# Optimization experiments

Measured on AMD Instinct MI355X. Metric: run time of the kernel, lower is better.

## Reference

```python
import jax, jax.numpy as jnp
import numpy as np

D = 64        # inner_feature_len (dim)
HID = 128     # hidden_channels of the edge MLP
NCONV = 2     # n_conv
STEPS = 3     # Set2Set processing_steps
NSEG = 128    # number of graphs in the batch


def setup_inputs() -> dict:
    key = jax.random.key(0)
    ks = jax.random.split(key, 30)
    N, E, FN, FE = 10000, 64000, 92, 41
    s = 0.05
    p = lambda i, shape: jax.random.normal(ks[i], shape, jnp.float32) * s
    return {
        "x": jax.random.normal(ks[0], (N, FN), jnp.float32),
        "edge_attr": jax.random.uniform(ks[1], (E, FE), dtype=jnp.float32),
        "lin0_w": p(2, (D, FN)), "lin0_b": p(3, (D,)),
        "nn1_w": p(4, (HID, FE)), "nn1_b": p(5, (HID,)),
        "nn2_w": p(6, (D * D, HID)), "nn2_b": p(7, (D * D,)),
        "root_w": p(8, (D, D)), "conv_b": p(9, (D,)),
        "gru_w_ih": p(10, (3 * D, D)), "gru_w_hh": p(11, (3 * D, D)),
        "gru_b_ih": p(12, (3 * D,)), "gru_b_hh": p(13, (3 * D,)),
        "lstm_w_ih": p(14, (4 * D, 2 * D)), "lstm_w_hh": p(15, (4 * D, D)),
        "lstm_b_ih": p(16, (4 * D,)), "lstm_b_hh": p(17, (4 * D,)),
        "lin1_w": p(18, (D, 2 * D)), "lin1_b": p(19, (D,)),
        "lin2_w": p(20, (1, D)), "lin2_b": p(21, (1,)),
        "edge_index": jax.random.randint(ks[22], (2, E), 0, N, dtype=jnp.int32),
        "batch": jnp.sort(jax.random.randint(ks[23], (N,), 0, NSEG, dtype=jnp.int32)),
    }


def _gru_step(m, h, w_ih, w_hh, b_ih, b_hh):
    # torch GRU gate order: r, z, n
    gi = m @ w_ih.T + b_ih
    gh = h @ w_hh.T + b_hh
    r = jax.nn.sigmoid(gi[:, :D] + gh[:, :D])
    z = jax.nn.sigmoid(gi[:, D:2 * D] + gh[:, D:2 * D])
    n = jnp.tanh(gi[:, 2 * D:] + r * gh[:, 2 * D:])
    return (1.0 - z) * n + z * h


def _forward(x, edge_attr, lin0_w, lin0_b, nn1_w, nn1_b, nn2_w, nn2_b, root_w, conv_b,
             gru_w_ih, gru_w_hh, gru_b_ih, gru_b_hh, lstm_w_ih, lstm_w_hh, lstm_b_ih,
             lstm_b_hh, lin1_w, lin1_b, lin2_w, lin2_b, edge_index, batch):
    N = x.shape[0]
    src, dst = edge_index[0], edge_index[1]

    # Edge-conditioned weight matrices: [E, D, D] (dominant intermediate)
    We = (jax.nn.relu(edge_attr @ nn1_w.T + nn1_b) @ nn2_w.T + nn2_b).reshape(-1, D, D)
    deg = jnp.clip(jax.ops.segment_sum(jnp.ones_like(src, jnp.float32), dst, num_segments=N), 1.0, None)

    out = jax.nn.relu(x @ lin0_w.T + lin0_b)   # [N, D]
    h = out                                     # GRU hidden (num_layers=1)
    for _ in range(NCONV):
        # NNConv: gather -> per-edge matmul -> scatter-mean, plus root transform + bias
        msg = jnp.einsum('ei,eio->eo', out[src], We)                 # [E, D]
        agg = jax.ops.segment_sum(msg, dst, num_segments=N) / deg[:, None]
        m = jax.nn.relu(agg + out @ root_w.T + conv_b)
        h = _gru_step(m, h, gru_w_ih, gru_w_hh, gru_b_ih, gru_b_hh)
        out = h

    # Set2Set pooling (LSTM-attention readout)
    q_star = jnp.zeros((NSEG, 2 * D), x.dtype)
    hl = jnp.zeros((NSEG, D), x.dtype)
    cl = jnp.zeros((NSEG, D), x.dtype)
    for _ in range(STEPS):
        g = q_star @ lstm_w_ih.T + lstm_b_ih + hl @ lstm_w_hh.T + lstm_b_hh
        i = jax.nn.sigmoid(g[:, :D])
        f = jax.nn.sigmoid(g[:, D:2 * D])
        gg = jnp.tanh(g[:, 2 * D:3 * D])
        o = jax.nn.sigmoid(g[:, 3 * D:])
        cl = f * cl + i * gg
        hl = o * jnp.tanh(cl)
        q = hl                                   # [NSEG, D]
        e = jnp.sum(out * q[batch], axis=-1)     # [N]
        mmax = jax.ops.segment_max(e, batch, num_segments=NSEG)
        a = jnp.exp(e - mmax[batch])
        denom = jax.ops.segment_sum(a, batch, num_segments=NSEG)
        a = a / denom[batch]
        r = jax.ops.segment_sum(a[:, None] * out, batch, num_segments=NSEG)  # [NSEG, D]
        q_star = jnp.concatenate([q, r], axis=1)

    y = jax.nn.relu(q_star @ lin1_w.T + lin1_b) @ lin2_w.T + lin2_b
    return y.reshape(-1)


def reference(x, edge_attr, lin0_w, lin0_b, nn1_w, nn1_b, nn2_w, nn2_b, root_w, conv_b,
              gru_w_ih, gru_w_hh, gru_b_ih, gru_b_hh, lstm_w_ih, lstm_w_hh, lstm_b_ih,
              lstm_b_hh, lin1_w, lin1_b, lin2_w, lin2_b, edge_index, batch):
    return _forward(x, edge_attr, lin0_w, lin0_b, nn1_w, nn1_b, nn2_w, nn2_b, root_w,
                    conv_b, gru_w_ih, gru_w_hh, gru_b_ih, gru_b_hh, lstm_w_ih, lstm_w_hh,
                    lstm_b_ih, lstm_b_hh, lin1_w, lin1_b, lin2_w, lin2_b, edge_index, batch)
```

## Files before the change

### kernel.cpp

```cpp
#include <hip/hip_runtime.h>
#include <hip/hip_bf16.h>
#include <math.h>

#define DD 64
#define HIDC 128
#define FN 92
#define FE 41
#define S2CAP 192

typedef unsigned short u16;
typedef short bf16x8 __attribute__((ext_vector_type(8)));
typedef float f32x4 __attribute__((ext_vector_type(4)));

__device__ __forceinline__ float sigmoidf_(float x){ return 1.f/(1.f+expf(-x)); }

__device__ __forceinline__ u16 f2bf(float v){
  union { float f; unsigned u; } x; x.f = v;
  unsigned r = x.u + 0x7fff + ((x.u >> 16) & 1);
  return (u16)(r >> 16);
}
__device__ __forceinline__ float bf2f(u16 v){
  union { float f; unsigned u; } x; x.u = ((unsigned)v) << 16;
  return x.f;
}
__device__ __forceinline__ void split_bf(float v, u16& h, u16& l){
  h = f2bf(v); l = f2bf(v - bf2f(h));
}

__global__ void k_pack(const float* __restrict__ lin0_w, const float* __restrict__ nn1_w,
                       const float* __restrict__ root_w, const float* __restrict__ gwih,
                       const float* __restrict__ gwhh, const float* __restrict__ lwih,
                       const float* __restrict__ lwhh, const float* __restrict__ lin1_w,
                       float* __restrict__ lin0T, float* __restrict__ nn1T,
                       float* __restrict__ rootT, float* __restrict__ wihT,
                       float* __restrict__ whhT, float* __restrict__ lwihT,
                       float* __restrict__ lwhhT, float* __restrict__ lin1T)
{
  int idx = blockIdx.x*blockDim.x + threadIdx.x;
  if (idx < 92*64){ int k=idx/64, o=idx%64; lin0T[k*64+o] = lin0_w[o*92+k]; return; } idx -= 92*64;
  if (idx < 41*128){ int k=idx/128, h=idx%128; nn1T[k*128+h] = nn1_w[h*41+k]; return; } idx -= 41*128;
  if (idx < 64*64){ int i=idx/64, o=idx%64; rootT[i*64+o] = root_w[o*64+i]; return; } idx -= 64*64;
  if (idx < 64*192){ int i=idx/192, g=idx%192; wihT[i*192+g] = gwih[g*64+i]; return; } idx -= 64*192;
  if (idx < 64*192){ int i=idx/192, g=idx%192; whhT[i*192+g] = gwhh[g*64+i]; return; } idx -= 64*192;
  if (idx < 128*256){ int j=idx/256, t=idx%256; lwihT[j*256+t] = lwih[t*128+j]; return; } idx -= 128*256;
  if (idx < 64*256){ int j=idx/256, t=idx%256; lwhhT[j*256+t] = lwhh[t*64+j]; return; } idx -= 64*256;
  if (idx < 128*64){ int j=idx/64, t=idx%64; lin1T[j*64+t] = lin1_w[t*128+j]; return; }
}

__global__ void k_pack_b2(const float* __restrict__ nn2_w,
                          u16* __restrict__ BhT, u16* __restrict__ BlT){
  int idx = blockIdx.x*256 + threadIdx.x;
  if (idx >= 524288) return;
  int i  = idx & 63;
  int ho = (idx >> 6) & 4095;
  int c  = idx >> 18;
  int h = ho >> 6, o = ho & 63;
  float v = nn2_w[(size_t)(i*64+o)*128 + c*64 + h];
  u16 hi, lo; split_bf(v, hi, lo);
  BhT[idx] = hi; BlT[idx] = lo;
}

__global__ void k_pack_b1(const float* __restrict__ nn1_w,
                          u16* __restrict__ BT1h, u16* __restrict__ BT1l){
  int idx = blockIdx.x*256 + threadIdx.x;
  if (idx >= 8192) return;
  int h = idx >> 6, k = idx & 63;
  float v = (k < FE) ? nn1_w[(size_t)h*FE + k] : 0.f;
  u16 hi, lo; split_bf(v, hi, lo);
  BT1h[idx] = hi; BT1l[idx] = lo;
}

__global__ void k_split_ea(const float* __restrict__ ea, const int* __restrict__ sortedE,
                           u16* __restrict__ eaH, u16* __restrict__ eaL, int E){
  int idx = blockIdx.x*256 + threadIdx.x;
  if (idx >= E*64) return;
  int ew = idx >> 6, k = idx & 63;
  int e = sortedE[ew];
  float v = (k < FE) ? ea[(size_t)e*FE + k] : 0.f;
  u16 hi, lo; split_bf(v, hi, lo);
  eaH[idx] = hi; eaL[idx] = lo;
}

__global__ __launch_bounds__(256) void k_node_mlp(const float* __restrict__ x,
    const float* __restrict__ lin0T, const float* __restrict__ lin0_b,
    const float* __restrict__ nn2_b,
    float* __restrict__ out, u16* __restrict__ outH, u16* __restrict__ outL,
    float* __restrict__ bterm, int N)
{
  __shared__ float xs[4][FN];
  int base = blockIdx.x*4;
  for (int i=threadIdx.x; i<4*FN; i+=256){
    int n = base + i/FN;
    xs[i/FN][i%FN] = (n<N) ? x[(size_t)n*FN + i%FN] : 0.f;
  }
  __syncthreads();
  int ln = threadIdx.x>>6, o = threadIdx.x&63;
  int n = base+ln;
  if (n>=N) return;
  float acc = lin0_b[o];
  #pragma unroll 4
  for (int k=0;k<FN;k++) acc = fmaf(xs[ln][k], lin0T[k*64+o], acc);
  float v = fmaxf(acc, 0.f);
  out[(size_t)n*64+o] = v;
  u16 hi, lo; split_bf(v, hi, lo);
  outH[(size_t)n*64+o] = hi;
  outL[(size_t)n*64+o] = lo;
  float bt = 0.f;
  #pragma unroll 8
  for (int i=0;i<64;i++) bt = fmaf(__shfl(v, i, 64), nn2_b[i*64+o], bt);
  bterm[(size_t)n*64+o] = bt;
}

__global__ void k_count(const int* __restrict__ dst, const int* __restrict__ src,
                        float* __restrict__ deg, int* __restrict__ scnt, int E){
  int e = blockIdx.x*blockDim.x + threadIdx.x;
  if (e < E){
    atomicAdd(&deg[dst[e]], 1.f);
    atomicAdd(&scnt[src[e]], 1);
  }
}

__global__ void k_scan1(const int* __restrict__ cnt, int* __restrict__ excl,
                        int* __restrict__ bsum, int N){
  __shared__ int buf[256];
  int i = blockIdx.x*256 + threadIdx.x;
  int v = (i<N) ? cnt[i] : 0;
  buf[threadIdx.x] = v;
  __syncthreads();
  #pragma unroll
  for (int off=1; off<256; off<<=1){
    int t = (threadIdx.x>=off) ? buf[threadIdx.x-off] : 0;
    __syncthreads();
    buf[threadIdx.x] += t;
    __syncthreads();
  }
  if (i<N) excl[i] = buf[threadIdx.x] - v;
  if (threadIdx.x==255) bsum[blockIdx.x] = buf[255];
}
__global__ void k_scan2(int* __restrict__ bsum, int nb){
  __shared__ int buf[256];
  int v = (threadIdx.x<nb) ? bsum[threadIdx.x] : 0;
  buf[threadIdx.x] = v;
  __syncthreads();
  #pragma unroll
  for (int off=1; off<256; off<<=1){
    int t = (threadIdx.x>=off) ? buf[threadIdx.x-off] : 0;
    __syncthreads();
    buf[threadIdx.x] += t;
    __syncthreads();
  }
  if (threadIdx.x<nb) bsum[threadIdx.x] = buf[threadIdx.x] - v;
}
__global__ void k_scan3(int* __restrict__ starts, int* __restrict__ cursor,
                        const int* __restrict__ bsum, int N, int E){
  int i = blockIdx.x*256 + threadIdx.x;
  if (i<N){
    int s = starts[i] + bsum[blockIdx.x];
    starts[i] = s;
    cursor[i] = s;
  }
  if (i==0) starts[N] = E;
}

__global__ void k_sort(const int* __restrict__ src, const int* __restrict__ dst,
                       int* __restrict__ cursor, int* __restrict__ sortedE,
                       int* __restrict__ srcS, int* __restrict__ dstS, int E){
  int e = blockIdx.x*256 + threadIdx.x;
  if (e < E){
    int s = src[e];
    int p = atomicAdd(&cursor[s], 1);
    sortedE[p] = e;
    srcS[p] = s;
    dstS[p] = dst[e];
  }
}

__global__ __launch_bounds__(256,3) void k_edge_mlp_mfma(
    const u16* __restrict__ eaH, const u16* __restrict__ eaL,
    const u16* __restrict__ BT1h, const u16* __restrict__ BT1l,
    const float* __restrict__ nn1_b, float* __restrict__ hidden, int E)
{
  const int lane = threadIdx.x & 63;
  const int wave = threadIdx.x >> 6;
  const int row  = lane & 15;
  const int quad = lane >> 4;
  const int m0 = blockIdx.x*128 + (wave>>1)*64;
  const int n0 = (wave&1)*64;

  bf16x8 AH0[4], AH1[4], AL0[4], AL1[4];
  #pragma unroll
  for (int p=0;p<4;p++){
    int ar = min(m0 + p*16 + row, E-1);
    const u16* aH = eaH + (size_t)ar*64 + quad*8;
    const u16* aL = eaL + (size_t)ar*64 + quad*8;
    AH0[p] = *(const bf16x8*)(aH);
    AH1[p] = *(const bf16x8*)(aH + 32);
    AL0[p] = *(const bf16x8*)(aL);
    AL1[p] = *(const bf16x8*)(aL + 32);
  }
  #pragma unroll
  for (int tb=0;tb<4;tb++){
    const u16* bH = BT1h + (size_t)(n0 + tb*16 + row)*64 + quad*8;
    const u16* bL = BT1l + (size_t)(n0 + tb*16 + row)*64 + quad*8;
    bf16x8 bh0 = *(const bf16x8*)(bH);
    bf16x8 bh1 = *(const bf16x8*)(bH + 32);
    bf16x8 bl0 = *(const bf16x8*)(bL);
    bf16x8 bl1 = *(const bf16x8*)(bL + 32);
    float4 bias;
    {
      int nb = n0 + tb*16 + quad*4;
      bias.x = nn1_b[nb+0]; bias.y = nn1_b[nb+1];
      bias.z = nn1_b[nb+2]; bias.w = nn1_b[nb+3];
    }
    #pragma unroll
    for (int ta=0;ta<4;ta++){
      f32x4 a = {0.f,0.f,0.f,0.f};
      a = __builtin_amdgcn_mfma_f32_16x16x32_bf16(bh0, AH0[ta], a, 0,0,0);
      a = __builtin_amdgcn_mfma_f32_16x16x32_bf16(bh1, AH1[ta], a, 0,0,0);
      a = __builtin_amdgcn_mfma_f32_16x16x32_bf16(bl0, AH0[ta], a, 0,0,0);
      a = __builtin_amdgcn_mfma_f32_16x16x32_bf16(bl1, AH1[ta], a, 0,0,0);
      a = __builtin_amdgcn_mfma_f32_16x16x32_bf16(bh0, AL0[ta], a, 0,0,0);
      a = __builtin_amdgcn_mfma_f32_16x16x32_bf16(bh1, AL1[ta], a, 0,0,0);
      int m = m0 + ta*16 + row;
      if (m < E){
        float4 v;
        v.x = fmaxf(a[0]+bias.x, 0.f); v.y = fmaxf(a[1]+bias.y, 0.f);
        v.z = fmaxf(a[2]+bias.z, 0.f); v.w = fmaxf(a[3]+bias.w, 0.f);
        *(float4*)(hidden + (size_t)m*128 + n0 + tb*16 + quad*4) = v;
      }
    }
  }
}

__global__ __launch_bounds__(256,3) void k_qgemm_mfma(
    const u16* __restrict__ Ah, const u16* __restrict__ Al,
    const u16* __restrict__ BhT, const u16* __restrict__ BlT,
    u16* __restrict__ C, int M)
{
  const int lane = threadIdx.x & 63;
  const int wave = threadIdx.x >> 6;
  const int row  = lane & 15;
  const int quad = lane >> 4;
  const int m0 = blockIdx.y * 64;
  const int n0 = blockIdx.x * 256 + wave * 64;

  bf16x8 AH0[4], AH1[4], AL0[4], AL1[4];
  #pragma unroll
  for (int p=0;p<4;p++){
    int ar = min(m0 + p*16 + row, M-1);
    const u16* aH = Ah + (size_t)ar*64 + quad*8;
    const u16* aL = Al + (size_t)ar*64 + quad*8;
    AH0[p] = *(const bf16x8*)(aH);
    AH1[p] = *(const bf16x8*)(aH + 32);
    AL0[p] = *(const bf16x8*)(aL);
    AL1[p] = *(const bf16x8*)(aL + 32);
  }

  #pragma unroll
  for (int tb=0;tb<4;tb++){
    const u16* bH = BhT + (size_t)(n0 + tb*16 + row)*64 + quad*8;
    const u16* bL = BlT + (size_t)(n0 + tb*16 + row)*64 + quad*8;
    bf16x8 bh0 = *(const bf16x8*)(bH);
    bf16x8 bh1 = *(const bf16x8*)(bH + 32);
    bf16x8 bl0 = *(const bf16x8*)(bL);
    bf16x8 bl1 = *(const bf16x8*)(bL + 32);
    #pragma unroll
    for (int ta=0;ta<4;ta++){
      f32x4 a = {0.f,0.f,0.f,0.f};
      a = __builtin_amdgcn_mfma_f32_16x16x32_bf16(bh0, AH0[ta], a, 0,0,0);
      a = __builtin_amdgcn_mfma_f32_16x16x32_bf16(bh1, AH1[ta], a, 0,0,0);
      a = __builtin_amdgcn_mfma_f32_16x16x32_bf16(bl0, AH0[ta], a, 0,0,0);
      a = __builtin_amdgcn_mfma_f32_16x16x32_bf16(bl1, AH1[ta], a, 0,0,0);
      a = __builtin_amdgcn_mfma_f32_16x16x32_bf16(bh0, AL0[ta], a, 0,0,0);
      a = __builtin_amdgcn_mfma_f32_16x16x32_bf16(bh1, AL1[ta], a, 0,0,0);
      int m = m0 + ta*16 + row;
      if (m < M){
        ushort4 v;
        v.x = f2bf(a[0]); v.y = f2bf(a[1]); v.z = f2bf(a[2]); v.w = f2bf(a[3]);
        *(ushort4*)(C + (size_t)m*4096 + n0 + tb*16 + quad*4) = v;
      }
    }
  }
}

template<int PASS>
__global__ __launch_bounds__(256) void k_edge_gather(const u16* __restrict__ Q,
    const float* __restrict__ hidden, int h0,
    const float* __restrict__ bterm, const int* __restrict__ srcS,
    const int* __restrict__ dstS,
    float* __restrict__ msg, float* __restrict__ agg, int E)
{
  __shared__ float hs[4][2][64];
  __shared__ float red[4][2][64];
  const int wv = threadIdx.x>>6, lane = threadIdx.x&63;
  const int ew0 = (blockIdx.x*4 + wv)*2;
  const bool v0 = (ew0 < E), v1 = (ew0+1 < E);
  const int e0 = v0 ? ew0 : 0;
  const int e1 = v1 ? ew0+1 : 0;
  const int s0 = srcS[e0], s1 = srcS[e1];
  hs[wv][0][lane] = hidden[(size_t)e0*128 + h0 + lane];
  hs[wv][1][lane] = hidden[(size_t)e1*128 + h0 + lane];
  const int sg = lane>>4, oq = lane&15;
  const u16* q0 = Q + (size_t)s0*4096 + sg*64 + oq*4;
  const u16* q1 = Q + (size_t)s1*4096 + sg*64 + oq*4;
  float a00=0.f,a01=0.f,a02=0.f,a03=0.f;
  float a10=0.f,a11=0.f,a12=0.f,a13=0.f;
  #pragma unroll
  for (int j=0;j<16;j++){
    ushort4 qa = *(const ushort4*)(q0 + j*256);
    ushort4 qb = *(const ushort4*)(q1 + j*256);
    float h0v = hs[wv][0][j*4 + sg];
    float h1v = hs[wv][1][j*4 + sg];
    a00 = fmaf(h0v, bf2f(qa.x), a00); a01 = fmaf(h0v, bf2f(qa.y), a01);
    a02 = fmaf(h0v, bf2f(qa.z), a02); a03 = fmaf(h0v, bf2f(qa.w), a03);
    a10 = fmaf(h1v, bf2f(qb.x), a10); a11 = fmaf(h1v, bf2f(qb.y), a11);
    a12 = fmaf(h1v, bf2f(qb.z), a12); a13 = fmaf(h1v, bf2f(qb.w), a13);
  }
  a00 += __shfl_xor(a00,16); a00 += __shfl_xor(a00,32);
  a01 += __shfl_xor(a01,16); a01 += __shfl_xor(a01,32);
  a02 += __shfl_xor(a02,16); a02 += __shfl_xor(a02,32);
  a03 += __shfl_xor(a03,16); a03 += __shfl_xor(a03,32);
  a10 += __shfl_xor(a10,16); a10 += __shfl_xor(a10,32);
  a11 += __shfl_xor(a11,16); a11 += __shfl_xor(a11,32);
  a12 += __shfl_xor(a12,16); a12 += __shfl_xor(a12,32);
  a13 += __shfl_xor(a13,16); a13 += __shfl_xor(a13,32);
  if (lane < 16){
    float4 r0; r0.x=a00; r0.y=a01; r0.z=a02; r0.w=a03;
    float4 r1; r1.x=a10; r1.y=a11; r1.z=a12; r1.w=a13;
    *(float4*)&red[wv][0][lane*4] = r0;
    *(float4*)&red[wv][1][lane*4] = r1;
  }
  if (v0){
    float rv = red[wv][0][lane];
    if (PASS == 0) msg[(size_t)ew0*64 + lane] = bterm[(size_t)s0*64 + lane] + rv;
    else atomicAdd(&agg[(size_t)dstS[ew0]*64 + lane], msg[(size_t)ew0*64 + lane] + rv);
  }
  if (v1){
    float rv = red[wv][1][lane];
    if (PASS == 0) msg[(size_t)(ew0+1)*64 + lane] = bterm[(size_t)s1*64 + lane] + rv;
    else atomicAdd(&agg[(size_t)dstS[ew0+1]*64 + lane], msg[(size_t)(ew0+1)*64 + lane] + rv);
  }
}

__global__ __launch_bounds__(256) void k_node_update(const float* __restrict__ outOld,
    const float* __restrict__ agg, const float* __restrict__ deg,
    const float* __restrict__ rootT, const float* __restrict__ conv_b,
    const float* __restrict__ wihT, const float* __restrict__ whhT,
    const float* __restrict__ b_ih, const float* __restrict__ b_hh,
    const float* __restrict__ nn2_b,
    float* __restrict__ outNew, u16* __restrict__ outH, u16* __restrict__ outL,
    float* __restrict__ bterm, int N)
{
  __shared__ float hs[4][64];
  __shared__ float ms[4][64];
  int ln = threadIdx.x>>6, o = threadIdx.x&63;
  int n = blockIdx.x*4+ln;
  bool ok = (n<N);
  float h = ok ? outOld[(size_t)n*64+o] : 0.f;
  hs[ln][o] = h;
  __syncthreads();
  float root = 0.f;
  #pragma unroll 8
  for (int i=0;i<64;i++) root = fmaf(hs[ln][i], rootT[i*64+o], root);
  float d = ok ? fmaxf(deg[n], 1.f) : 1.f;
  float a = ok ? agg[(size_t)n*64+o]/d : 0.f;
  float m = fmaxf(a + root + conv_b[o], 0.f);
  ms[ln][o] = m;
  __syncthreads();
  float gir=b_ih[o], giz=b_ih[64+o], gin=b_ih[128+o];
  float ghr=b_hh[o], ghz=b_hh[64+o], ghn=b_hh[128+o];
  #pragma unroll 4
  for (int i=0;i<64;i++){
    float mi = ms[ln][i], hi = hs[ln][i];
    gir = fmaf(mi, wihT[i*192+o],      gir);
    giz = fmaf(mi, wihT[i*192+64+o],   giz);
    gin = fmaf(mi, wihT[i*192+128+o],  gin);
    ghr = fmaf(hi, whhT[i*192+o],      ghr);
    ghz = fmaf(hi, whhT[i*192+64+o],   ghz);
    ghn = fmaf(hi, whhT[i*192+128+o],  ghn);
  }
  float r = sigmoidf_(gir+ghr);
  float z = sigmoidf_(giz+ghz);
  float nn = tanhf(gin + r*ghn);
  if (ok){
    float v = (1.f-z)*nn + z*h;
    outNew[(size_t)n*64+o] = v;
    u16 hi16, lo16; split_bf(v, hi16, lo16);
    outH[(size_t)n*64+o] = hi16;
    outL[(size_t)n*64+o] = lo16;
    float bt = 0.f;
    #pragma unroll 8
    for (int i=0;i<64;i++) bt = fmaf(__shfl(v, i, 64), nn2_b[i*64+o], bt);
    bterm[(size_t)n*64+o] = bt;
  }
}

__global__ __launch_bounds__(256) void k_set2set(const float* __restrict__ out,
    const int* __restrict__ batch, int N,
    const float* __restrict__ lwihT, const float* __restrict__ lwhhT,
    const float* __restrict__ b_ih, const float* __restrict__ b_hh,
    const float* __restrict__ lin1T, const float* __restrict__ lin1_b,
    const float* __restrict__ lin2_w, const float* __restrict__ lin2_b,
    float* __restrict__ y)
{
  __shared__ float X[S2CAP][65];
  __shared__ float earr[S2CAP];
  __shared__ float qstar[128], hl[64], cl[64], g[256];
  __shared__ float rpart[4][64], spart[4], redm[4], zs[64];
  __shared__ int sb[2];
  const int tid = threadIdx.x;
  const int b = blockIdx.x;
  const int wid = tid>>6, lane = tid&63;
  if (tid < 128) qstar[tid] = 0.f;
  if (tid < 64){ hl[tid]=0.f; cl[tid]=0.f; }
  if (tid == 0){
    int lo=0, hi=N;
    while (lo<hi){ int mid=(lo+hi)>>1; if (batch[mid] < b) lo=mid+1; else hi=mid; }
    sb[0]=lo;
    int lo2=lo, hi2=N;
    while (lo2<hi2){ int mid=(lo2+hi2)>>1; if (batch[mid] < b+1) lo2=mid+1; else hi2=mid; }
    sb[1]=lo2;
  }
  __syncthreads();
  const int nlo = sb[0], nhi = sb[1], nn = nhi - nlo;
  const bool single = (nn <= S2CAP);
  if (single){
    for (int idx = tid; idx < nn*64; idx += 256){
      X[idx>>6][idx&63] = out[(size_t)(nlo + (idx>>6))*64 + (idx&63)];
    }
  }
  __syncthreads();

  for (int step=0; step<3; step++){
    float gs = b_ih[tid] + b_hh[tid];
    for (int j=0;j<128;j++) gs = fmaf(qstar[j], lwihT[j*256+tid], gs);
    for (int j=0;j<64;j++)  gs = fmaf(hl[j],    lwhhT[j*256+tid], gs);
    g[tid] = gs;
    __syncthreads();
    if (tid < 64){
      float ig = sigmoidf_(g[tid]);
      float fg = sigmoidf_(g[64+tid]);
      float gg = tanhf(g[128+tid]);
      float og = sigmoidf_(g[192+tid]);
      float c = fg*cl[tid] + ig*gg;
      cl[tid] = c;
      hl[tid] = og*tanhf(c);
    }
    __syncthreads();

    if (single){
      float lm = -INFINITY;
      for (int n = tid; n < nn; n += 256){
        float acc = 0.f;
        #pragma unroll 8
        for (int d=0; d<64; d++) acc = fmaf(X[n][d], hl[d], acc);
        earr[n] = acc;
        lm = fmaxf(lm, acc);
      }
      lm = fmaxf(lm, __shfl_xor(lm,1));  lm = fmaxf(lm, __shfl_xor(lm,2));
      lm = fmaxf(lm, __shfl_xor(lm,4));  lm = fmaxf(lm, __shfl_xor(lm,8));
      lm = fmaxf(lm, __shfl_xor(lm,16)); lm = fmaxf(lm, __shfl_xor(lm,32));
      if (lane==0) redm[wid] = lm;
      __syncthreads();
      if (tid==0) redm[0] = fmaxf(fmaxf(redm[0],redm[1]), fmaxf(redm[2],redm[3]));
      __syncthreads();
      const float gmax = redm[0];
      float ls = 0.f;
      for (int n = tid; n < nn; n += 256){
        float a = expf(earr[n] - gmax);
        earr[n] = a;
        ls += a;
      }
      ls += __shfl_xor(ls,1);  ls += __shfl_xor(ls,2);  ls += __shfl_xor(ls,4);
      ls += __shfl_xor(ls,8);  ls += __shfl_xor(ls,16); ls += __shfl_xor(ls,32);
      if (lane==0) spart[wid] = ls;
      __syncthreads();
      float racc = 0.f;
      for (int n = wid; n < nn; n += 4) racc = fmaf(earr[n], X[n][lane], racc);
      rpart[wid][lane] = racc;
      __syncthreads();
      if (tid < 64){
        float r = rpart[0][tid]+rpart[1][tid]+rpart[2][tid]+rpart[3][tid];
        float s = spart[0]+spart[1]+spart[2]+spart[3];
        qstar[tid] = hl[tid];
        qstar[64+tid] = (nn>0) ? r/s : 0.f;
      }
      __syncthreads();
    } else {
      float qv = hl[lane];
      float lm = -INFINITY;
      for (int n = nlo + wid; n < nhi; n += 4){
        float p = out[(size_t)n*64 + lane]*qv;
        p += __shfl_xor(p,1); p += __shfl_xor(p,2); p += __shfl_xor(p,4);
        p += __shfl_xor(p,8); p += __shfl_xor(p,16); p += __shfl_xor(p,32);
        lm = fmaxf(lm, p);
      }
      if (lane==0) redm[wid] = lm;
      __syncthreads();
      if (tid==0) redm[0] = fmaxf(fmaxf(redm[0],redm[1]), fmaxf(redm[2],redm[3]));
      __syncthreads();
      float gmax = redm[0];
      float sw = 0.f, racc = 0.f;
      for (int n = nlo + wid; n < nhi; n += 4){
        float ol = out[(size_t)n*64 + lane];
        float p = ol*qv;
        p += __shfl_xor(p,1); p += __shfl_xor(p,2); p += __shfl_xor(p,4);
        p += __shfl_xor(p,8); p += __shfl_xor(p,16); p += __shfl_xor(p,32);
        float a = expf(p - gmax);
        sw += a;
        racc = fmaf(a, ol, racc);
      }
      rpart[wid][lane] = racc;
      if (lane==0) spart[wid] = sw;
      __syncthreads();
      if (tid < 64){
        float r = rpart[0][tid]+rpart[1][tid]+rpart[2][tid]+rpart[3][tid];
        float s = spart[0]+spart[1]+spart[2]+spart[3];
        qstar[tid] = hl[tid];
        qstar[64+tid] = (nn>0) ? r/s : 0.f;
      }
      __syncthreads();
    }
  }
  if (tid < 64){
    float acc = lin1_b[tid];
    for (int j=0;j<128;j++) acc = fmaf(qstar[j], lin1T[j*64+tid], acc);
    zs[tid] = fmaxf(acc, 0.f);
  }
  __syncthreads();
  if (tid < 64){
    float v = zs[lane]*lin2_w[lane];
    v += __shfl_xor(v,1); v += __shfl_xor(v,2); v += __shfl_xor(v,4);
    v += __shfl_xor(v,8); v += __shfl_xor(v,16); v += __shfl_xor(v,32);
    if (lane==0) y[b] = v + lin2_b[0];
  }
}

extern "C" void kernel_launch(void* const* d_in, const int* in_sizes, int n_in,
                              void* d_out, int out_size, void* d_ws, size_t ws_size,
                              hipStream_t stream)
{
  const float* x      = (const float*)d_in[0];
  const float* eattr  = (const float*)d_in[1];
  const float* lin0_w = (const float*)d_in[2];
  const float* lin0_b = (const float*)d_in[3];
  const float* nn1_w  = (const float*)d_in[4];
  const float* nn1_b  = (const float*)d_in[5];
  const float* nn2_w  = (const float*)d_in[6];
  const float* nn2_b  = (const float*)d_in[7];
  const float* root_w = (const float*)d_in[8];
  const float* conv_b = (const float*)d_in[9];
  const float* gwih   = (const float*)d_in[10];
  const float* gwhh   = (const float*)d_in[11];
  const float* gbih   = (const float*)d_in[12];
  const float* gbhh   = (const float*)d_in[13];
  const float* lwih   = (const float*)d_in[14];
  const float* lwhh   = (const float*)d_in[15];
  const float* lbih   = (const float*)d_in[16];
  const float* lbhh   = (const float*)d_in[17];
  const float* lin1_w = (const float*)d_in[18];
  const float* lin1_b = (const float*)d_in[19];
  const float* lin2_w = (const float*)d_in[20];
  const float* lin2_b = (const float*)d_in[21];
  const int*   eidx   = (const int*)d_in[22];
  const int*   batch  = (const int*)d_in[23];

  const int N = in_sizes[0]/FN;
  const int E = in_sizes[1]/FE;
  const int* srcI = eidx;
  const int* dstI = eidx + E;

  char* w = (char*)d_ws;
  size_t off = 0;
  auto alloc = [&](size_t bytes)->char* {
    char* p = w + off;
    off = (off + bytes + 255) & ~(size_t)255;
    return p;
  };
  float* degw  = (float*)alloc((size_t)N*4);
  int*   scnt  = (int*)alloc((size_t)N*4);
  int*   starts= (int*)alloc((size_t)(N+1)*4);
  int*   cursor= (int*)alloc((size_t)N*4);
  int*   bsum  = (int*)alloc((size_t)256*4);
  int*   sortedE=(int*)alloc((size_t)E*4);
  int*   srcS  = (int*)alloc((size_t)E*4);
  int*   dstS  = (int*)alloc((size_t)E*4);
  float* outA  = (float*)alloc((size_t)N*64*4);
  float* outB  = (float*)alloc((size_t)N*64*4);
  u16*   outAH = (u16*)alloc((size_t)N*64*2);
  u16*   outAL = (u16*)alloc((size_t)N*64*2);
  u16*   outBH = (u16*)alloc((size_t)N*64*2);
  u16*   outBL = (u16*)alloc((size_t)N*64*2);
  float* agg   = (float*)alloc((size_t)N*64*4);
  float* bterm = (float*)alloc((size_t)N*64*4);
  float* hidden= (float*)alloc((size_t)E*128*4);
  float* msg   = (float*)alloc((size_t)E*64*4);
  u16*   B2hT  = (u16*)alloc((size_t)524288*2);
  u16*   B2lT  = (u16*)alloc((size_t)524288*2);
  u16*   BT1h  = (u16*)alloc((size_t)8192*2);
  u16*   BT1l  = (u16*)alloc((size_t)8192*2);
  float* lin0T = (float*)alloc((size_t)92*64*4);
  float* nn1T  = (float*)alloc((size_t)41*128*4);
  float* rootT = (float*)alloc((size_t)64*64*4);
  float* wihT  = (float*)alloc((size_t)64*192*4);
  float* whhT  = (float*)alloc((size_t)64*192*4);
  float* lwihT = (float*)alloc((size_t)128*256*4);
  float* lwhhT = (float*)alloc((size_t)64*256*4);
  float* lin1T = (float*)alloc((size_t)128*64*4);
  u16*   Q     = (u16*)alloc((size_t)N*4096*2);
  u16* eaH = (u16*)Q;
  u16* eaL = eaH + (size_t)E*64;

  const int NB = (N+255)/256;

  hipMemsetAsync(degw, 0, (size_t)N*4, stream);
  hipMemsetAsync(scnt, 0, (size_t)N*4, stream);
  k_pack<<<(97152+255)/256, 256, 0, stream>>>(lin0_w, nn1_w, root_w, gwih, gwhh,
      lwih, lwhh, lin1_w, lin0T, nn1T, rootT, wihT, whhT, lwihT, lwhhT, lin1T);
  k_pack_b2<<<524288/256, 256, 0, stream>>>(nn2_w, B2hT, B2lT);
  k_pack_b1<<<8192/256, 256, 0, stream>>>(nn1_w, BT1h, BT1l);
  k_node_mlp<<<(N+3)/4, 256, 0, stream>>>(x, lin0T, lin0_b, nn2_b, outA, outAH, outAL, bterm, N);
  k_count<<<(E+255)/256, 256, 0, stream>>>(dstI, srcI, degw, scnt, E);
  k_scan1<<<NB, 256, 0, stream>>>(scnt, starts, bsum, N);
  k_scan2<<<1, 256, 0, stream>>>(bsum, NB);
  k_scan3<<<NB, 256, 0, stream>>>(starts, cursor, bsum, N, E);
  k_sort<<<(E+255)/256, 256, 0, stream>>>(srcI, dstI, cursor, sortedE, srcS, dstS, E);
  k_split_ea<<<((size_t)E*64+255)/256, 256, 0, stream>>>(eattr, sortedE, eaH, eaL, E);
  k_edge_mlp_mfma<<<(E+127)/128, 256, 0, stream>>>(eaH, eaL, BT1h, BT1l, nn1_b, hidden, E);

  float* cur = outA; float* nxt = outB;
  u16* curH = outAH; u16* curL = outAL;
  u16* nxtH = outBH; u16* nxtL = outBL;
  const dim3 qgrid(16, (N+63)/64);
  const int gatherGx = (E+7)/8;
  for (int conv=0; conv<2; conv++){
    hipMemsetAsync(agg, 0, (size_t)N*64*4, stream);
    k_qgemm_mfma<<<qgrid, 256, 0, stream>>>(curH, curL, B2hT, B2lT, Q, N);
    k_edge_gather<0><<<gatherGx, 256, 0, stream>>>(Q, hidden, 0, bterm, srcS, dstS, msg, agg, E);
    k_qgemm_mfma<<<qgrid, 256, 0, stream>>>(curH, curL, B2hT + 262144, B2lT + 262144, Q, N);
    k_edge_gather<1><<<gatherGx, 256, 0, stream>>>(Q, hidden, 64, bterm, srcS, dstS, msg, agg, E);
    k_node_update<<<(N+3)/4, 256, 0, stream>>>(cur, agg, degw, rootT, conv_b,
        wihT, whhT, gbih, gbhh, nn2_b, nxt, nxtH, nxtL, bterm, N);
    float* t = cur; cur = nxt; nxt = t;
    u16* th = curH; curH = nxtH; nxtH = th;
    u16* tl = curL; curL = nxtL; nxtL = tl;
  }

  k_set2set<<<128, 256, 0, stream>>>(cur, batch, N, lwihT, lwhhT, lbih, lbhh,
      lin1T, lin1_b, lin2_w, lin2_b, (float*)d_out);
}
```

Before: 633.7 us.

## Fuse per-node Q GEMM with edge gather into one source-blocked conv kernel

Replaces the two Q-GEMM plus two edge-gather passes per conv with one kernel. It takes blocks of 16 source nodes, computes their Q slices on the fly with MFMA into shared memory, and contracts them with the hidden activations of edges sorted by source, then atomically adds into agg. The hidden buffer is stored transposed so edge chunks can be read with coalesced loads. This removes the large N×4096 bf16 Q intermediate and the msg buffer round trip through global memory. In exchange, each block recomputes Q for all 128 hidden channels, synchronises twice per channel group, and runs at lower occupancy; hidden is now written with strided stores.

```diff
diff --git a/kernel.cpp b/kernel.cpp
--- a/kernel.cpp
+++ b/kernel.cpp
@@ -7,10 +7,14 @@
 #define FN 92
 #define FE 41
 #define S2CAP 192
+#define NPB 16
+#define ECW 32
+#define ECB 128
 
 typedef unsigned short u16;
 typedef short bf16x8 __attribute__((ext_vector_type(8)));
 typedef float f32x4 __attribute__((ext_vector_type(4)));
+typedef u16 u16x8 __attribute__((ext_vector_type(8)));
 
 __device__ __forceinline__ float sigmoidf_(float x){ return 1.f/(1.f+expf(-x)); }
 
@@ -178,7 +182,7 @@
 __global__ __launch_bounds__(256,3) void k_edge_mlp_mfma(
     const u16* __restrict__ eaH, const u16* __restrict__ eaL,
     const u16* __restrict__ BT1h, const u16* __restrict__ BT1l,
-    const float* __restrict__ nn1_b, float* __restrict__ hidden, int E)
+    const float* __restrict__ nn1_b, float* __restrict__ hiddenT, int E)
 {
   const int lane = threadIdx.x & 63;
   const int wave = threadIdx.x >> 6;
@@ -223,122 +227,117 @@
       a = __builtin_amdgcn_mfma_f32_16x16x32_bf16(bh1, AL1[ta], a, 0,0,0);
       int m = m0 + ta*16 + row;
       if (m < E){
-        float4 v;
-        v.x = fmaxf(a[0]+bias.x, 0.f); v.y = fmaxf(a[1]+bias.y, 0.f);
-        v.z = fmaxf(a[2]+bias.z, 0.f); v.w = fmaxf(a[3]+bias.w, 0.f);
-        *(float4*)(hidden + (size_t)m*128 + n0 + tb*16 + quad*4) = v;
+        int colb = n0 + tb*16 + quad*4;
+        hiddenT[(size_t)(colb+0)*E + m] = fmaxf(a[0]+bias.x, 0.f);
+        hiddenT[(size_t)(colb+1)*E + m] = fmaxf(a[1]+bias.y, 0.f);
+        hiddenT[(size_t)(colb+2)*E + m] = fmaxf(a[2]+bias.z, 0.f);
+        hiddenT[(size_t)(colb+3)*E + m] = fmaxf(a[3]+bias.w, 0.f);
       }
     }
   }
 }
 
-__global__ __launch_bounds__(256,3) void k_qgemm_mfma(
+__global__ __launch_bounds__(256,2) void k_fused_conv(
     const u16* __restrict__ Ah, const u16* __restrict__ Al,
     const u16* __restrict__ BhT, const u16* __restrict__ BlT,
-    u16* __restrict__ C, int M)
+    const float* __restrict__ hiddenT, const float* __restrict__ bterm,
+    const int* __restrict__ starts, const int* __restrict__ srcS,
+    const int* __restrict__ dstS, float* __restrict__ agg, int N, int E)
 {
-  const int lane = threadIdx.x & 63;
-  const int wave = threadIdx.x >> 6;
-  const int row  = lane & 15;
-  const int quad = lane >> 4;
-  const int m0 = blockIdx.y * 64;
-  const int n0 = blockIdx.x * 256 + wave * 64;
-
-  bf16x8 AH0[4], AH1[4], AL0[4], AL1[4];
-  #pragma unroll
-  for (int p=0;p<4;p++){
-    int ar = min(m0 + p*16 + row, M-1);
+  __shared__ float Qs[4][16][68];
+  __shared__ float hst[4][ECB];
+  const int tid = threadIdx.x;
+  const int wv = tid >> 6, lane = tid & 63;
+  const int row = lane & 15, quad = lane >> 4;
+  const int n0g = blockIdx.x * NPB;
+  if (n0g >= N) return;
+
+  bf16x8 AH0, AH1, AL0, AL1;
+  {
+    int ar = min(n0g + row, N-1);
     const u16* aH = Ah + (size_t)ar*64 + quad*8;
     const u16* aL = Al + (size_t)ar*64 + quad*8;
-    AH0[p] = *(const bf16x8*)(aH);
-    AH1[p] = *(const bf16x8*)(aH + 32);
-    AL0[p] = *(const bf16x8*)(aL);
-    AL1[p] = *(const bf16x8*)(aL + 32);
-  }
-
-  #pragma unroll
-  for (int tb=0;tb<4;tb++){
-    const u16* bH = BhT + (size_t)(n0 + tb*16 + row)*64 + quad*8;
-    const u16* bL = BlT + (size_t)(n0 + tb*16 + row)*64 + quad*8;
-    bf16x8 bh0 = *(const bf16x8*)(bH);
-    bf16x8 bh1 = *(const bf16x8*)(bH + 32);
-    bf16x8 bl0 = *(const bf16x8*)(bL);
-    bf16x8 bl1 = *(const bf16x8*)(bL + 32);
+    AH0 = *(const bf16x8*)(aH);
+    AH1 = *(const bf16x8*)(aH + 32);
+    AL0 = *(const bf16x8*)(aL);
+    AL1 = *(const bf16x8*)(aL + 32);
+  }
+
+  const int eblk0 = starts[n0g];
+  const int eblk1 = starts[min(n0g + NPB, N)];
+
+  const int j0 = tid >> 7,        el0 = tid & 127;
+  const int j1 = (tid+256) >> 7,  el1 = (tid+256) & 127;
+
+  for (int ce0 = eblk0; ce0 < eblk1; ce0 += ECB){
+    const int cnt = min(ECB, eblk1 - ce0);
+    const int myE0 = ce0 + wv*ECW;
+    const int nE = min(max(ce0 + cnt - myE0, 0), ECW);
+    int sv = 0;
+    if (lane < nE) sv = srcS[myE0 + lane] - n0g;
+    float macc[ECW];
     #pragma unroll
-    for (int ta=0;ta<4;ta++){
-      f32x4 a = {0.f,0.f,0.f,0.f};
-      a = __builtin_amdgcn_mfma_f32_16x16x32_bf16(bh0, AH0[ta], a, 0,0,0);
-      a = __builtin_amdgcn_mfma_f32_16x16x32_bf16(bh1, AH1[ta], a, 0,0,0);
-      a = __builtin_amdgcn_mfma_f32_16x16x32_bf16(bl0, AH0[ta], a, 0,0,0);
-      a = __builtin_amdgcn_mfma_f32_16x16x32_bf16(bl1, AH1[ta], a, 0,0,0);
-      a = __builtin_amdgcn_mfma_f32_16x16x32_bf16(bh0, AL0[ta], a, 0,0,0);
-      a = __builtin_amdgcn_mfma_f32_16x16x32_bf16(bh1, AL1[ta], a, 0,0,0);
-      int m = m0 + ta*16 + row;
-      if (m < M){
-        ushort4 v;
-        v.x = f2bf(a[0]); v.y = f2bf(a[1]); v.z = f2bf(a[2]); v.w = f2bf(a[3]);
-        *(ushort4*)(C + (size_t)m*4096 + n0 + tb*16 + quad*4) = v;
+    for (int k=0;k<ECW;k++) macc[k] = 0.f;
+
+    for (int g=0; g<32; ++g){
+      float hr0 = (el0 < cnt) ? hiddenT[(size_t)(g*4+j0)*E + ce0 + el0] : 0.f;
+      float hr1 = (el1 < cnt) ? hiddenT[(size_t)(g*4+j1)*E + ce0 + el1] : 0.f;
+      const int cb = g*4 + wv;
+      const u16* Bh = BhT + ((size_t)(cb>>6))*262144 + (size_t)(cb&63)*4096;
+      const u16* Bl = BlT + ((size_t)(cb>>6))*262144 + (size_t)(cb&63)*4096;
+      f32x4 acc[4];
+      #pragma unroll
+      for (int tb=0;tb<4;tb++) acc[tb] = (f32x4){0.f,0.f,0.f,0.f};
+      #pragma unroll
+      for (int tb=0;tb<4;tb++){
+        const u16* bH = Bh + (size_t)(tb*16 + row)*64 + quad*8;
+        const u16* bL = Bl + (size_t)(tb*16 + row)*64 + quad*8;
+        bf16x8 bh0 = *(const bf16x8*)(bH);
+        bf16x8 bh1 = *(const bf16x8*)(bH + 32);
+        bf16x8 bl0 = *(const bf16x8*)(bL);
+        bf16x8 bl1 = *(const bf16x8*)(bL + 32);
+        f32x4 a = acc[tb];
+        a = __builtin_amdgcn_mfma_f32_16x16x32_bf16(bh0, AH0, a, 0,0,0);
+        a = __builtin_amdgcn_mfma_f32_16x16x32_bf16(bh1, AH1, a, 0,0,0);
+        a = __builtin_amdgcn_mfma_f32_16x16x32_bf16(bl0, AH0, a, 0,0,0);
+        a = __builtin_amdgcn_mfma_f32_16x16x32_bf16(bl1, AH1, a, 0,0,0);
+        a = __builtin_amdgcn_mfma_f32_16x16x32_bf16(bh0, AL0, a, 0,0,0);
+        a = __builtin_amdgcn_mfma_f32_16x16x32_bf16(bh1, AL1, a, 0,0,0);
+        acc[tb] = a;
+      }
+      __syncthreads();
+      #pragma unroll
+      for (int tb=0;tb<4;tb++)
+        *(f32x4*)&Qs[wv][row][tb*16+quad*4] = acc[tb];
+      hst[j0][el0] = hr0;
+      hst[j1][el1] = hr1;
+      __syncthreads();
+      #pragma unroll
+      for (int k=0;k<ECW;k++){
+        if (k < nE){
+          const int slk = __builtin_amdgcn_readlane(sv, k);
+          const int el = wv*ECW + k;
+          float m = macc[k];
+          m = fmaf(hst[0][el], Qs[0][slk][lane], m);
+          m = fmaf(hst[1][el], Qs[1][slk][lane], m);
+          m = fmaf(hst[2][el], Qs[2][slk][lane], m);
+          m = fmaf(hst[3][el], Qs[3][slk][lane], m);
+          macc[k] = m;
+        }
       }
     }
-  }
-}
-
-template<int PASS>
-__global__ __launch_bounds__(256) void k_edge_gather(const u16* __restrict__ Q,
-    const float* __restrict__ hidden, int h0,
-    const float* __restrict__ bterm, const int* __restrict__ srcS,
-    const int* __restrict__ dstS,
-    float* __restrict__ msg, float* __restrict__ agg, int E)
-{
-  __shared__ float hs[4][2][64];
-  __shared__ float red[4][2][64];
-  const int wv = threadIdx.x>>6, lane = threadIdx.x&63;
-  const int ew0 = (blockIdx.x*4 + wv)*2;
-  const bool v0 = (ew0 < E), v1 = (ew0+1 < E);
-  const int e0 = v0 ? ew0 : 0;
-  const int e1 = v1 ? ew0+1 : 0;
-  const int s0 = srcS[e0], s1 = srcS[e1];
-  hs[wv][0][lane] = hidden[(size_t)e0*128 + h0 + lane];
-  hs[wv][1][lane] = hidden[(size_t)e1*128 + h0 + lane];
-  const int sg = lane>>4, oq = lane&15;
-  const u16* q0 = Q + (size_t)s0*4096 + sg*64 + oq*4;
-  const u16* q1 = Q + (size_t)s1*4096 + sg*64 + oq*4;
-  float a00=0.f,a01=0.f,a02=0.f,a03=0.f;
-  float a10=0.f,a11=0.f,a12=0.f,a13=0.f;
-  #pragma unroll
-  for (int j=0;j<16;j++){
-    ushort4 qa = *(const ushort4*)(q0 + j*256);
-    ushort4 qb = *(const ushort4*)(q1 + j*256);
-    float h0v = hs[wv][0][j*4 + sg];
-    float h1v = hs[wv][1][j*4 + sg];
-    a00 = fmaf(h0v, bf2f(qa.x), a00); a01 = fmaf(h0v, bf2f(qa.y), a01);
-    a02 = fmaf(h0v, bf2f(qa.z), a02); a03 = fmaf(h0v, bf2f(qa.w), a03);
-    a10 = fmaf(h1v, bf2f(qb.x), a10); a11 = fmaf(h1v, bf2f(qb.y), a11);
-    a12 = fmaf(h1v, bf2f(qb.z), a12); a13 = fmaf(h1v, bf2f(qb.w), a13);
-  }
-  a00 += __shfl_xor(a00,16); a00 += __shfl_xor(a00,32);
-  a01 += __shfl_xor(a01,16); a01 += __shfl_xor(a01,32);
-  a02 += __shfl_xor(a02,16); a02 += __shfl_xor(a02,32);
-  a03 += __shfl_xor(a03,16); a03 += __shfl_xor(a03,32);
-  a10 += __shfl_xor(a10,16); a10 += __shfl_xor(a10,32);
-  a11 += __shfl_xor(a11,16); a11 += __shfl_xor(a11,32);
-  a12 += __shfl_xor(a12,16); a12 += __shfl_xor(a12,32);
-  a13 += __shfl_xor(a13,16); a13 += __shfl_xor(a13,32);
-  if (lane < 16){
-    float4 r0; r0.x=a00; r0.y=a01; r0.z=a02; r0.w=a03;
-    float4 r1; r1.x=a10; r1.y=a11; r1.z=a12; r1.w=a13;
-    *(float4*)&red[wv][0][lane*4] = r0;
-    *(float4*)&red[wv][1][lane*4] = r1;
-  }
-  if (v0){
-    float rv = red[wv][0][lane];
-    if (PASS == 0) msg[(size_t)ew0*64 + lane] = bterm[(size_t)s0*64 + lane] + rv;
-    else atomicAdd(&agg[(size_t)dstS[ew0]*64 + lane], msg[(size_t)ew0*64 + lane] + rv);
-  }
-  if (v1){
-    float rv = red[wv][1][lane];
-    if (PASS == 0) msg[(size_t)(ew0+1)*64 + lane] = bterm[(size_t)s1*64 + lane] + rv;
-    else atomicAdd(&agg[(size_t)dstS[ew0+1]*64 + lane], msg[(size_t)(ew0+1)*64 + lane] + rv);
+    int dv = 0;
+    if (lane < nE) dv = dstS[myE0 + lane];
+    #pragma unroll
+    for (int k=0;k<ECW;k++){
+      if (k < nE){
+        const int slk = __builtin_amdgcn_readlane(sv, k);
+        const int dk  = __builtin_amdgcn_readlane(dv, k);
+        const float bt = bterm[(size_t)(n0g + slk)*64 + lane];
+        atomicAdd(&agg[(size_t)dk*64 + lane], macc[k] + bt);
+      }
+    }
+    __syncthreads();
   }
 }
 
@@ -593,8 +592,9 @@
   u16*   outBL = (u16*)alloc((size_t)N*64*2);
   float* agg   = (float*)alloc((size_t)N*64*4);
   float* bterm = (float*)alloc((size_t)N*64*4);
-  float* hidden= (float*)alloc((size_t)E*128*4);
-  float* msg   = (float*)alloc((size_t)E*64*4);
+  float* hiddenT=(float*)alloc((size_t)E*128*4);
+  u16*   eaH   = (u16*)alloc((size_t)E*64*2);
+  u16*   eaL   = (u16*)alloc((size_t)E*64*2);
   u16*   B2hT  = (u16*)alloc((size_t)524288*2);
   u16*   B2lT  = (u16*)alloc((size_t)524288*2);
   u16*   BT1h  = (u16*)alloc((size_t)8192*2);
@@ -607,9 +607,6 @@
   float* lwihT = (float*)alloc((size_t)128*256*4);
   float* lwhhT = (float*)alloc((size_t)64*256*4);
   float* lin1T = (float*)alloc((size_t)128*64*4);
-  u16*   Q     = (u16*)alloc((size_t)N*4096*2);
-  u16* eaH = (u16*)Q;
-  u16* eaL = eaH + (size_t)E*64;
 
   const int NB = (N+255)/256;
 
@@ -626,19 +623,16 @@
   k_scan3<<<NB, 256, 0, stream>>>(starts, cursor, bsum, N, E);
   k_sort<<<(E+255)/256, 256, 0, stream>>>(srcI, dstI, cursor, sortedE, srcS, dstS, E);
   k_split_ea<<<((size_t)E*64+255)/256, 256, 0, stream>>>(eattr, sortedE, eaH, eaL, E);
-  k_edge_mlp_mfma<<<(E+127)/128, 256, 0, stream>>>(eaH, eaL, BT1h, BT1l, nn1_b, hidden, E);
+  k_edge_mlp_mfma<<<(E+127)/128, 256, 0, stream>>>(eaH, eaL, BT1h, BT1l, nn1_b, hiddenT, E);
 
   float* cur = outA; float* nxt = outB;
   u16* curH = outAH; u16* curL = outAL;
   u16* nxtH = outBH; u16* nxtL = outBL;
-  const dim3 qgrid(16, (N+63)/64);
-  const int gatherGx = (E+7)/8;
+  const int fusedG = (N + NPB - 1) / NPB;
   for (int conv=0; conv<2; conv++){
     hipMemsetAsync(agg, 0, (size_t)N*64*4, stream);
-    k_qgemm_mfma<<<qgrid, 256, 0, stream>>>(curH, curL, B2hT, B2lT, Q, N);
-    k_edge_gather<0><<<gatherGx, 256, 0, stream>>>(Q, hidden, 0, bterm, srcS, dstS, msg, agg, E);
-    k_qgemm_mfma<<<qgrid, 256, 0, stream>>>(curH, curL, B2hT + 262144, B2lT + 262144, Q, N);
-    k_edge_gather<1><<<gatherGx, 256, 0, stream>>>(Q, hidden, 64, bterm, srcS, dstS, msg, agg, E);
+    k_fused_conv<<<fusedG, 256, 0, stream>>>(curH, curL, B2hT, B2lT, hiddenT,
+        bterm, starts, srcS, dstS, agg, N, E);
     k_node_update<<<(N+3)/4, 256, 0, stream>>>(cur, agg, degw, rootT, conv_b,
         wihT, whhT, gbih, gbhh, nn2_b, nxt, nxtH, nxtL, bterm, N);
     float* t = cur; cur = nxt; nxt = t;
```

Measured after the change: 857.2 us. +35.3%, slower.
